# Performance work log

Hardware: AMD Instinct MI355X
Metric: run time of the kernel (lower is better)

The kernel has to match this reference:

```python
import jax, jax.numpy as jnp
import numpy as np
import math

EMBED_DIM = 1024
NUM_HEADS = 16
HEAD_DIM = EMBED_DIM // NUM_HEADS          # 64
SUB_HEAD_DIM = HEAD_DIM // 2               # 32
SCALING = 1.0 / math.sqrt(SUB_HEAD_DIM)
LAMBDA_INIT = 0.8 - 0.6 * math.exp(-0.3 * 0)  # layer_idx = 0 -> 0.2


def setup_inputs() -> dict:
    key = jax.random.key(0)
    ks = jax.random.split(key, 10)
    B, T, D = 2, 2048, EMBED_DIM
    xav = math.sqrt(6.0 / (D + D))  # xavier_uniform bound for square-ish mats
    return {
        "query": jax.random.normal(ks[0], (B, T, D), jnp.float32),
        "key": jax.random.normal(ks[1], (B, T, D), jnp.float32),
        "value": jax.random.normal(ks[2], (B, T, D), jnp.float32),
        "in_proj_weight": jax.random.uniform(ks[3], (3 * D, D), jnp.float32, -xav, xav),
        "in_proj_bias": jnp.zeros((3 * D,), jnp.float32),
        "out_proj_weight": jax.random.uniform(ks[4], (D, D), jnp.float32, -xav, xav),
        "out_proj_bias": jnp.zeros((D,), jnp.float32),
        "lambda_q1": 0.1 * jax.random.normal(ks[5], (SUB_HEAD_DIM,), jnp.float32),
        "lambda_k1": 0.1 * jax.random.normal(ks[6], (SUB_HEAD_DIM,), jnp.float32),
        "lambda_q2": 0.1 * jax.random.normal(ks[7], (SUB_HEAD_DIM,), jnp.float32),
        "lambda_k2": 0.1 * jax.random.normal(ks[8], (SUB_HEAD_DIM,), jnp.float32),
    }


def reference(query, key, value, in_proj_weight, in_proj_bias,
              out_proj_weight, out_proj_bias,
              lambda_q1, lambda_k1, lambda_q2, lambda_k2):
    B, T, D = query.shape
    S = key.shape[1]
    H, hd, sd = NUM_HEADS, HEAD_DIM, SUB_HEAD_DIM

    qw, kw, vw = jnp.split(in_proj_weight, 3, axis=0)
    qb, kb, vb = jnp.split(in_proj_bias, 3, axis=0)
    q = query @ qw.T + qb
    k = key @ kw.T + kb
    v = value @ vw.T + vb

    # [B, H, T, head_dim]
    q = q.reshape(B, T, H, hd).transpose(0, 2, 1, 3)
    k = k.reshape(B, S, H, hd).transpose(0, 2, 1, 3)
    v = v.reshape(B, S, H, hd).transpose(0, 2, 1, 3)

    q1, q2 = q[..., :sd], q[..., sd:]
    k1, k2 = k[..., :sd], k[..., sd:]

    logits_1 = jnp.einsum('bhtd,bhsd->bhts', q1, k1) * SCALING
    logits_2 = jnp.einsum('bhtd,bhsd->bhts', q2, k2) * SCALING

    a1 = jax.nn.softmax(logits_1, axis=-1)
    a2 = jax.nn.softmax(logits_2, axis=-1)

    lam = (jnp.exp(jnp.dot(lambda_q1, lambda_k1))
           - jnp.exp(jnp.dot(lambda_q2, lambda_k2)) + LAMBDA_INIT)

    diff_weights = a1 - lam * a2
    attn_output = jnp.einsum('bhts,bhsd->bhtd', diff_weights, v)
    attn_output = attn_output * (1.0 - LAMBDA_INIT)

    attn_output = attn_output.transpose(0, 2, 1, 3).reshape(B, T, D)
    output = attn_output @ out_proj_weight.T + out_proj_bias
    return output
```

## Files before the change

kernel.cpp:

```cpp
#include <hip/hip_runtime.h>
#include <cstdint>
#include <cstddef>

typedef unsigned short u16;
typedef __attribute__((ext_vector_type(8))) short bf16x8;
typedef __attribute__((ext_vector_type(4))) short bf16x4;
typedef __attribute__((ext_vector_type(4))) float f32x4;

__device__ __forceinline__ u16 f2bf(float f) {
  uint32_t u = __float_as_uint(f);
  u += 0x7fffu + ((u >> 16) & 1u);
  return (u16)(u >> 16);
}

__device__ __forceinline__ short f2bfs(float f) {
  __bf16 h = (__bf16)f;
  return __builtin_bit_cast(short, h);
}

__device__ __forceinline__ float bf2f(u16 u) {
  return __uint_as_float(((uint32_t)u) << 16);
}

#define MFMA16(a, b, c) __builtin_amdgcn_mfma_f32_16x16x32_bf16((a), (b), (c), 0, 0, 0)

__device__ __forceinline__ float ex2(float x) {
#if __has_builtin(__builtin_amdgcn_exp2f)
  return __builtin_amdgcn_exp2f(x);
#else
  return exp2f(x);
#endif
}

__global__ __launch_bounds__(256) void cvt3_kernel(const float* __restrict__ q,
                                                   const float* __restrict__ k,
                                                   const float* __restrict__ v,
                                                   u16* __restrict__ out, int n8) {
  int i = blockIdx.x * blockDim.x + threadIdx.x;
  if (i >= n8) return;
  const float* src = blockIdx.y == 0 ? q : (blockIdx.y == 1 ? k : v);
  u16* dst = out + (size_t)blockIdx.y * n8 * 8;
  const float4* p = (const float4*)src;
  float4 a = p[i * 2], b = p[i * 2 + 1];
  u16 o[8] = {f2bf(a.x), f2bf(a.y), f2bf(a.z), f2bf(a.w),
              f2bf(b.x), f2bf(b.y), f2bf(b.z), f2bf(b.w)};
  *(int4*)(dst + (size_t)i * 8) = *(const int4*)o;
}

__global__ __launch_bounds__(256) void cvtw_kernel(const float* __restrict__ w0,
                                                   const float* __restrict__ w1,
                                                   u16* __restrict__ o0,
                                                   u16* __restrict__ o1,
                                                   int n8_0, int n8_1) {
  int i = blockIdx.x * blockDim.x + threadIdx.x;
  const float* src;
  u16* dst;
  if (blockIdx.y == 0) {
    if (i >= n8_0) return;
    src = w0; dst = o0;
  } else {
    if (i >= n8_1) return;
    src = w1; dst = o1;
  }
  const float4* p = (const float4*)src;
  float4 a = p[i * 2], b = p[i * 2 + 1];
  u16 o[8] = {f2bf(a.x), f2bf(a.y), f2bf(a.z), f2bf(a.w),
              f2bf(b.x), f2bf(b.y), f2bf(b.z), f2bf(b.w)};
  *(int4*)(dst + (size_t)i * 8) = *(const int4*)o;
}

template <typename OUT_T, bool SPLIT_A>
__global__ __launch_bounds__(256) void gemm_bt(const u16* __restrict__ Abase,
                                               const u16* __restrict__ B,
                                               const float* __restrict__ bias,
                                               OUT_T* __restrict__ C,
                                               u16* __restrict__ QH, u16* __restrict__ KH,
                                               u16* __restrict__ VT,
                                               int M, int N, int K) {
  __shared__ u16 As[128][68];
  __shared__ u16 Bs[128][68];
  const int nb = blockIdx.x, mb = blockIdx.y;
  const int t = threadIdx.x;
  const u16* A = Abase + (SPLIT_A ? (size_t)(nb >> 3) * (size_t)M * K : (size_t)0);
  const int w = t >> 6, lane = t & 63;
  const int wr = w >> 1, wc = w & 1;
  const int lr = lane & 15, lk = lane >> 4;
  const f32x4 zero4 = {0.f, 0.f, 0.f, 0.f};
  f32x4 acc[4][4];
#pragma unroll
  for (int i = 0; i < 4; ++i)
#pragma unroll
    for (int j = 0; j < 4; ++j) acc[i][j] = zero4;

  const int srow = t >> 3;
  const int scol = (t & 7) << 3;
  const u16* Ap = A + (size_t)(mb * 128 + srow) * K + scol;
  const u16* Bp = B + (size_t)(nb * 128 + srow) * K + scol;

  for (int k0 = 0; k0 < K; k0 += 64) {
    __syncthreads();
#pragma unroll
    for (int j = 0; j < 4; ++j) {
      *(int4*)&As[srow + 32 * j][scol] = *(const int4*)(Ap + (size_t)(32 * j) * K + k0);
      *(int4*)&Bs[srow + 32 * j][scol] = *(const int4*)(Bp + (size_t)(32 * j) * K + k0);
    }
    __syncthreads();
#pragma unroll
    for (int kk = 0; kk < 2; ++kk) {
      bf16x8 af[4], bfr[4];
#pragma unroll
      for (int mf = 0; mf < 4; ++mf)
        af[mf] = *(const bf16x8*)&As[wr * 64 + mf * 16 + lr][kk * 32 + lk * 8];
#pragma unroll
      for (int nf = 0; nf < 4; ++nf)
        bfr[nf] = *(const bf16x8*)&Bs[wc * 64 + nf * 16 + lr][kk * 32 + lk * 8];
#pragma unroll
      for (int mf = 0; mf < 4; ++mf)
#pragma unroll
        for (int nf = 0; nf < 4; ++nf) acc[mf][nf] = MFMA16(af[mf], bfr[nf], acc[mf][nf]);
    }
  }

  if constexpr (SPLIT_A) {
    const int third = nb >> 3;
    const int bb = mb >> 4;
#pragma unroll
    for (int nf = 0; nf < 4; ++nf) {
      const int col = nb * 128 + wc * 64 + nf * 16 + lr;
      const int c = col & 1023;
      const int h = c >> 6, d = c & 63;
      const float bv = bias[col];
      u16* qk = (third == 0 ? QH : KH) + (size_t)(bb * 16 + h) * 2048 * 64;
      u16* vt = VT + ((size_t)(bb * 16 + h) * 64 + d) * 2048;
#pragma unroll
      for (int mf = 0; mf < 4; ++mf) {
        const int row0 = mb * 128 + wr * 64 + mf * 16 + lk * 4;
        const int s0 = row0 & 2047;
        if (third < 2) {
#pragma unroll
          for (int r = 0; r < 4; ++r)
            qk[(size_t)(s0 + r) * 64 + d] = f2bf(acc[mf][nf][r] + bv);
        } else {
          u16 tmp[4];
#pragma unroll
          for (int r = 0; r < 4; ++r) tmp[r] = f2bf(acc[mf][nf][r] + bv);
          *(uint2*)&vt[s0] = *(const uint2*)tmp;
        }
      }
    }
  } else {
#pragma unroll
    for (int nf = 0; nf < 4; ++nf) {
      const int col = nb * 128 + wc * 64 + nf * 16 + lr;
      const float bv = bias[col];
#pragma unroll
      for (int mf = 0; mf < 4; ++mf) {
        const int row0 = mb * 128 + wr * 64 + mf * 16 + lk * 4;
#pragma unroll
        for (int r = 0; r < 4; ++r)
          ((float*)C)[(size_t)(row0 + r) * N + col] = acc[mf][nf][r] + bv;
      }
    }
  }
}

__global__ __launch_bounds__(256, 4) void diff_attn(const u16* __restrict__ QH,
                                                    const u16* __restrict__ KH,
                                                    const u16* __restrict__ VT,
                                                    const float* __restrict__ lq1,
                                                    const float* __restrict__ lk1,
                                                    const float* __restrict__ lq2,
                                                    const float* __restrict__ lk2,
                                                    u16* __restrict__ ATTN) {
  __shared__ u16 Ks[64][68];
  __shared__ u16 Vs[64][68];
  const int t = threadIdx.x;
  const int id = blockIdx.x;
  const int swz = (id & 7) * 128 + (id >> 3);
  const int qt = swz & 31, bh = swz >> 5;
  const int b = bh >> 4, h = bh & 15;
  const int w = t >> 6, lane = t & 63;
  const int lr = lane & 15, lk = lane >> 4;
  const float QSC = 0.17677669529663687f * 1.4426950408889634f;

  float dd1 = 0.f, dd2 = 0.f;
  for (int i = 0; i < 32; ++i) { dd1 += lq1[i] * lk1[i]; dd2 += lq2[i] * lk2[i]; }
  const float lam = __expf(dd1) - __expf(dd2) + 0.2f;

  const int srow = t >> 3;
  const int scol = (t & 7) << 3;
  const int krow = ((srow & 4) << 2) | ((srow & 24) >> 1) | (srow & 3);
  const u16* qh = QH + (size_t)(b * 16 + h) * 2048 * 64;
  const u16* kh = KH + (size_t)(b * 16 + h) * 2048 * 64;
  const u16* vt = VT + (size_t)(b * 16 + h) * 64 * 2048;

  bf16x8 qa[2];
#pragma unroll
  for (int hh = 0; hh < 2; ++hh) {
    bf16x8 q = *(const bf16x8*)(qh + (size_t)(qt * 64 + w * 16 + lr) * 64 + hh * 32 + lk * 8);
#pragma unroll
    for (int i = 0; i < 8; ++i) q[i] = f2bfs(bf2f((u16)q[i]) * QSC);
    qa[hh] = q;
  }

  const f32x4 zero4 = {0.f, 0.f, 0.f, 0.f};
  f32x4 O[2][4], Ol[2];
#pragma unroll
  for (int hh = 0; hh < 2; ++hh) {
    Ol[hh] = zero4;
#pragma unroll
    for (int df = 0; df < 4; ++df) O[hh][df] = zero4;
  }
  bf16x8 vone8;
#pragma unroll
  for (int i = 0; i < 8; ++i) vone8[i] = (short)0x3F80;

  const u16* kp0 = kh + (size_t)srow * 64 + scol;
  const u16* kp1 = kp0 + (size_t)32 * 64;
  const u16* vp0 = vt + (size_t)srow * 2048 + scol;
  const u16* vp1 = vp0 + (size_t)32 * 2048;

  int4 kA0 = *(const int4*)kp0;
  int4 kA1 = *(const int4*)kp1;
  int4 vA0 = *(const int4*)vp0;
  int4 vA1 = *(const int4*)vp1;
  int4 kB0, kB1, vB0, vB1;

  for (int it = 0; it < 32; ++it) {
    __syncthreads();
    *(int4*)&Ks[krow][scol]      = kA0;
    *(int4*)&Ks[krow + 32][scol] = kA1;
    *(int4*)&Vs[srow][scol]      = vA0;
    *(int4*)&Vs[srow + 32][scol] = vA1;
    if (it < 31) {
      const int s1 = (it + 1) * 64;
      kB0 = *(const int4*)(kp0 + (size_t)s1 * 64);
      kB1 = *(const int4*)(kp1 + (size_t)s1 * 64);
      vB0 = *(const int4*)(vp0 + s1);
      vB1 = *(const int4*)(vp1 + s1);
    }
    __syncthreads();

    bf16x8 pk8[2][2];
#pragma unroll
    for (int hh = 0; hh < 2; ++hh) {
      f32x4 St[4];
#pragma unroll
      for (int nf = 0; nf < 4; ++nf) {
        bf16x8 kb = *(const bf16x8*)&Ks[nf * 16 + lr][hh * 32 + lk * 8];
        St[nf] = MFMA16(kb, qa[hh], zero4);
      }
#pragma unroll
      for (int j = 0; j < 2; ++j) {
        bf16x8 p;
#pragma unroll
        for (int a = 0; a < 2; ++a)
#pragma unroll
          for (int r = 0; r < 4; ++r)
            p[a * 4 + r] = f2bfs(ex2(St[2 * j + a][r]));
        pk8[hh][j] = p;
      }
    }

    __builtin_amdgcn_s_setprio(1);
#pragma unroll
    for (int j = 0; j < 2; ++j) {
      const bf16x8 pa0 = pk8[0][j], pa1 = pk8[1][j];
#pragma unroll
      for (int df = 0; df < 4; ++df) {
        bf16x8 vb = *(const bf16x8*)&Vs[df * 16 + lr][j * 32 + lk * 8];
        O[0][df] = MFMA16(pa0, vb, O[0][df]);
        O[1][df] = MFMA16(pa1, vb, O[1][df]);
      }
      Ol[0] = MFMA16(pa0, vone8, Ol[0]);
      Ol[1] = MFMA16(pa1, vone8, Ol[1]);
    }
    __builtin_amdgcn_s_setprio(0);

    kA0 = kB0; kA1 = kB1; vA0 = vB0; vA1 = vB1;
  }

  float i1[4], i2[4];
#pragma unroll
  for (int r = 0; r < 4; ++r) {
    i1[r] = 1.f / Ol[0][r];
    i2[r] = 1.f / Ol[1][r];
  }
  const size_t qrow0 = (size_t)b * 2048 + (size_t)qt * 64;
#pragma unroll
  for (int df = 0; df < 4; ++df) {
    const int col = h * 64 + df * 16 + lr;
#pragma unroll
    for (int r = 0; r < 4; ++r) {
      const size_t row = qrow0 + w * 16 + lk * 4 + r;
      float v = 0.8f * (O[0][df][r] * i1[r] - lam * O[1][df][r] * i2[r]);
      ATTN[row * 1024 + col] = f2bf(v);
    }
  }
}

extern "C" void kernel_launch(void* const* d_in, const int* in_sizes, int n_in,
                              void* d_out, int out_size, void* d_ws, size_t ws_size,
                              hipStream_t stream) {
  (void)in_sizes; (void)n_in; (void)out_size; (void)ws_size;
  const float* query = (const float*)d_in[0];
  const float* key_  = (const float*)d_in[1];
  const float* value = (const float*)d_in[2];
  const float* ipw   = (const float*)d_in[3];
  const float* ipb   = (const float*)d_in[4];
  const float* opw   = (const float*)d_in[5];
  const float* opb   = (const float*)d_in[6];
  const float* lq1   = (const float*)d_in[7];
  const float* lk1   = (const float*)d_in[8];
  const float* lq2   = (const float*)d_in[9];
  const float* lk2   = (const float*)d_in[10];

  const int M = 4096, D = 1024;
  u16* X    = (u16*)d_ws;
  u16* Wqkv = X + (size_t)3 * M * D;
  u16* Wout = Wqkv + (size_t)3 * D * D;
  u16* QH   = Wout + (size_t)D * D;
  u16* KH   = QH + (size_t)M * D;
  u16* VT   = KH + (size_t)M * D;
  u16* ATTN = VT + (size_t)M * D;

  {
    int n8 = (int)((size_t)M * D / 8);
    cvt3_kernel<<<dim3((n8 + 255) / 256, 3), dim3(256), 0, stream>>>(
        query, key_, value, X, n8);
  }
  {
    int n8_0 = (int)((size_t)3 * D * D / 8);
    int n8_1 = (int)((size_t)D * D / 8);
    cvtw_kernel<<<dim3((n8_0 + 255) / 256, 2), dim3(256), 0, stream>>>(
        ipw, opw, Wqkv, Wout, n8_0, n8_1);
  }

  gemm_bt<u16, true><<<dim3(24, 32), dim3(256), 0, stream>>>(
      X, Wqkv, ipb, (u16*)nullptr, QH, KH, VT, M, 3 * D, D);
  diff_attn<<<dim3(1024), dim3(256), 0, stream>>>(QH, KH, VT, lq1, lk1, lq2, lk2, ATTN);
  gemm_bt<float, false><<<dim3(8, 32), dim3(256), 0, stream>>>(
      ATTN, Wout, opb, (float*)d_out, nullptr, nullptr, nullptr, M, D, D);
}
```

Before: 145.8 us.

## Double attention query tile to 128 rows with 512-thread blocks

Each attention block now runs 8 waves over 128 query rows instead of 4 waves over 64, and the grid is halved to 512 blocks. Each K/V tile in shared memory is reused by twice as many waves, and each thread loads one K and one V vector per tile instead of two. This halves global K/V traffic per query, in exchange for larger barrier groups and fewer blocks per CU (launch bounds go to 512,2), which may reduce latency hiding.

```diff
diff --git a/kernel.cpp b/kernel.cpp
--- a/kernel.cpp
+++ b/kernel.cpp
@@ -164,7 +164,7 @@
   }
 }
 
-__global__ __launch_bounds__(256, 4) void diff_attn(const u16* __restrict__ QH,
+__global__ __launch_bounds__(512, 2) void diff_attn(const u16* __restrict__ QH,
                                                     const u16* __restrict__ KH,
                                                     const u16* __restrict__ VT,
                                                     const float* __restrict__ lq1,
@@ -176,8 +176,8 @@
   __shared__ u16 Vs[64][68];
   const int t = threadIdx.x;
   const int id = blockIdx.x;
-  const int swz = (id & 7) * 128 + (id >> 3);
-  const int qt = swz & 31, bh = swz >> 5;
+  const int swz = (id & 7) * 64 + (id >> 3);
+  const int qt = swz & 15, bh = swz >> 4;
   const int b = bh >> 4, h = bh & 15;
   const int w = t >> 6, lane = t & 63;
   const int lr = lane & 15, lk = lane >> 4;
@@ -189,7 +189,7 @@
 
   const int srow = t >> 3;
   const int scol = (t & 7) << 3;
-  const int krow = ((srow & 4) << 2) | ((srow & 24) >> 1) | (srow & 3);
+  const int krow = (srow & 32) | ((srow & 4) << 2) | ((srow & 24) >> 1) | (srow & 3);
   const u16* qh = QH + (size_t)(b * 16 + h) * 2048 * 64;
   const u16* kh = KH + (size_t)(b * 16 + h) * 2048 * 64;
   const u16* vt = VT + (size_t)(b * 16 + h) * 64 * 2048;
@@ -197,7 +197,7 @@
   bf16x8 qa[2];
 #pragma unroll
   for (int hh = 0; hh < 2; ++hh) {
-    bf16x8 q = *(const bf16x8*)(qh + (size_t)(qt * 64 + w * 16 + lr) * 64 + hh * 32 + lk * 8);
+    bf16x8 q = *(const bf16x8*)(qh + (size_t)(qt * 128 + w * 16 + lr) * 64 + hh * 32 + lk * 8);
 #pragma unroll
     for (int i = 0; i < 8; ++i) q[i] = f2bfs(bf2f((u16)q[i]) * QSC);
     qa[hh] = q;
@@ -215,29 +215,21 @@
 #pragma unroll
   for (int i = 0; i < 8; ++i) vone8[i] = (short)0x3F80;
 
-  const u16* kp0 = kh + (size_t)srow * 64 + scol;
-  const u16* kp1 = kp0 + (size_t)32 * 64;
-  const u16* vp0 = vt + (size_t)srow * 2048 + scol;
-  const u16* vp1 = vp0 + (size_t)32 * 2048;
-
-  int4 kA0 = *(const int4*)kp0;
-  int4 kA1 = *(const int4*)kp1;
-  int4 vA0 = *(const int4*)vp0;
-  int4 vA1 = *(const int4*)vp1;
-  int4 kB0, kB1, vB0, vB1;
+  const u16* kp = kh + (size_t)srow * 64 + scol;
+  const u16* vp = vt + (size_t)srow * 2048 + scol;
+
+  int4 kA = *(const int4*)kp;
+  int4 vA = *(const int4*)vp;
+  int4 kB, vB;
 
   for (int it = 0; it < 32; ++it) {
     __syncthreads();
-    *(int4*)&Ks[krow][scol]      = kA0;
-    *(int4*)&Ks[krow + 32][scol] = kA1;
-    *(int4*)&Vs[srow][scol]      = vA0;
-    *(int4*)&Vs[srow + 32][scol] = vA1;
+    *(int4*)&Ks[krow][scol] = kA;
+    *(int4*)&Vs[srow][scol] = vA;
     if (it < 31) {
       const int s1 = (it + 1) * 64;
-      kB0 = *(const int4*)(kp0 + (size_t)s1 * 64);
-      kB1 = *(const int4*)(kp1 + (size_t)s1 * 64);
-      vB0 = *(const int4*)(vp0 + s1);
-      vB1 = *(const int4*)(vp1 + s1);
+      kB = *(const int4*)(kp + (size_t)s1 * 64);
+      vB = *(const int4*)(vp + s1);
     }
     __syncthreads();
 
@@ -277,7 +269,7 @@
     }
     __builtin_amdgcn_s_setprio(0);
 
-    kA0 = kB0; kA1 = kB1; vA0 = vB0; vA1 = vB1;
+    kA = kB; vA = vB;
   }
 
   float i1[4], i2[4];
@@ -286,7 +278,7 @@
     i1[r] = 1.f / Ol[0][r];
     i2[r] = 1.f / Ol[1][r];
   }
-  const size_t qrow0 = (size_t)b * 2048 + (size_t)qt * 64;
+  const size_t qrow0 = (size_t)b * 2048 + (size_t)qt * 128;
 #pragma unroll
   for (int df = 0; df < 4; ++df) {
     const int col = h * 64 + df * 16 + lr;
@@ -338,7 +330,7 @@
 
   gemm_bt<u16, true><<<dim3(24, 32), dim3(256), 0, stream>>>(
       X, Wqkv, ipb, (u16*)nullptr, QH, KH, VT, M, 3 * D, D);
-  diff_attn<<<dim3(1024), dim3(256), 0, stream>>>(QH, KH, VT, lq1, lk1, lq2, lk2, ATTN);
+  diff_attn<<<dim3(512), dim3(512), 0, stream>>>(QH, KH, VT, lq1, lk1, lq2, lk2, ATTN);
   gemm_bt<float, false><<<dim3(8, 32), dim3(256), 0, stream>>>(
       ATTN, Wout, opb, (float*)d_out, nullptr, nullptr, nullptr, M, D, D);
 }
```

After: 140.0 us. -4.0%, faster.
